# Optimization experiments

Hardware: AMD Instinct MI355X
Metric: run time of the kernel (lower is better)

## Reference

```python
import jax, jax.numpy as jnp
import numpy as np

EMB = 768
HEADS = 12
HEAD_DIM = EMB // HEADS

def setup_inputs() -> dict:
    key = jax.random.key(0)
    ks = jax.random.split(key, 5)
    B, T = 8, 1024
    x = jax.random.normal(ks[0], (B, T, EMB), dtype=jnp.float32)
    s = 1.0 / np.sqrt(EMB)
    W_attn = jax.random.normal(ks[1], (EMB, 3 * EMB), dtype=jnp.float32) * s
    b_attn = jax.random.normal(ks[2], (3 * EMB,), dtype=jnp.float32) * 0.02
    W_proj = jax.random.normal(ks[3], (EMB, EMB), dtype=jnp.float32) * s
    b_proj = jax.random.normal(ks[4], (EMB,), dtype=jnp.float32) * 0.02
    return {"x": x, "W_attn": W_attn, "b_attn": b_attn, "W_proj": W_proj, "b_proj": b_proj}

def reference(x, W_attn, b_attn, W_proj, b_proj):
    B, T, C = x.shape
    qkv = x @ W_attn + b_attn  # [B,T,3C]
    q, k, v = jnp.split(qkv, 3, axis=-1)
    # [B,H,T,d]
    q = q.reshape(B, T, HEADS, HEAD_DIM).transpose(0, 2, 1, 3)
    k = k.reshape(B, T, HEADS, HEAD_DIM).transpose(0, 2, 1, 3)
    v = v.reshape(B, T, HEADS, HEAD_DIM).transpose(0, 2, 1, 3)
    scores = jnp.einsum('bhqd,bhkd->bhqk', q, k) * (HEAD_DIM ** -0.5)
    causal = jnp.tril(jnp.ones((T, T), dtype=bool))
    scores = jnp.where(causal[None, None], scores, -jnp.inf)
    attn = jax.nn.softmax(scores, axis=-1)
    out = jnp.einsum('bhqk,bhkd->bhqd', attn, v)
    out = out.transpose(0, 2, 1, 3).reshape(B, T, C)
    return out @ W_proj + b_proj
```

## Files before the change

### kernel.cpp

```cpp
#include <hip/hip_runtime.h>
#include <hip/hip_bf16.h>
#include <math.h>

typedef __bf16 bf16;
typedef __attribute__((ext_vector_type(8))) __bf16 bf16x8;
typedef __attribute__((ext_vector_type(4))) short s16x4;
typedef __attribute__((ext_vector_type(4))) float f32x4;

#define EMB 768
#define T_SEQ 1024
#define HEADS 12
#define HDIM 64

__global__ void prep_k(const float* __restrict__ x, bf16* __restrict__ xb,
                       const float* __restrict__ Wa, bf16* __restrict__ Wta,
                       const float* __restrict__ Wp, bf16* __restrict__ Wtp) {
  __shared__ float tile[32][33];
  const int blk = blockIdx.x, tid = threadIdx.x;
  if (blk < 3072) {
    const size_t i = (size_t)blk * 256 + tid;
    const float4* p = (const float4*)(x + i * 8);
    const float4 a = p[0], b = p[1];
    bf16x8 v;
    v[0] = (bf16)a.x; v[1] = (bf16)a.y; v[2] = (bf16)a.z; v[3] = (bf16)a.w;
    v[4] = (bf16)b.x; v[5] = (bf16)b.y; v[6] = (bf16)b.z; v[7] = (bf16)b.w;
    *(bf16x8*)(xb + i * 8) = v;
    return;
  }
  const float* in;
  bf16* out;
  int C, t;
  if (blk < 3072 + 1728) { in = Wa; out = Wta; C = 3 * EMB; t = blk - 3072; }
  else                   { in = Wp; out = Wtp; C = EMB;     t = blk - 4800; }
  const int R = EMB;
  const int c0 = (t % (C / 32)) * 32, r0 = (t / (C / 32)) * 32;
  const int tx = tid & 31, ty = tid >> 5;
  for (int i = ty; i < 32; i += 8)
    tile[i][tx] = in[(size_t)(r0 + i) * C + c0 + tx];
  __syncthreads();
  for (int i = ty; i < 32; i += 8)
    out[(size_t)(c0 + i) * R + r0 + tx] = (bf16)tile[tx][i];
}

template <int MODE, int NXT>
__global__ __launch_bounds__(256) void gemm_bt(
    const bf16* __restrict__ A, const bf16* __restrict__ Bt, const float* __restrict__ bias,
    bf16* __restrict__ Cb, float* __restrict__ Cf, int M, int N, int K) {
  __shared__ __align__(16) bf16 As0[128 * 32];
  __shared__ __align__(16) bf16 As1[128 * 32];
  __shared__ __align__(16) bf16 Bs0[128 * 32];
  __shared__ __align__(16) bf16 Bs1[128 * 32];
  const int lane = threadIdx.x & 63;
  const int wave = threadIdx.x >> 6;
  const int quad = lane >> 4, lc = lane & 15;

  const int xcd = blockIdx.x & 7;
  const int idx = blockIdx.x >> 3;
  const int m0 = (xcd * 8 + (idx & 7)) * 128;
  const int n0 = (idx >> 3) * 128;

  const int wm = (wave >> 1) * 64, wn = (wave & 1) * 64;
  const int srow = lane >> 2;
  const int skk = (lane & 3) * 8;

  f32x4 zero = {0.f, 0.f, 0.f, 0.f};
  f32x4 acc[4][4];
#pragma unroll
  for (int i = 0; i < 4; ++i)
#pragma unroll
    for (int j = 0; j < 4; ++j) acc[i][j] = zero;

  for (int k0 = 0; k0 < K; k0 += 64) {
    __syncthreads();
#pragma unroll
    for (int c = wave; c < 8; c += 4) {
      const bf16* gA = A + (size_t)(m0 + c * 16 + srow) * K + k0 + skk;
      const bf16* gB = Bt + (size_t)(n0 + c * 16 + srow) * K + k0 + skk;
      __builtin_amdgcn_global_load_lds((const __attribute__((address_space(1))) void*)gA,
                                       (__attribute__((address_space(3))) void*)(As0 + c * 512), 16, 0, 0);
      __builtin_amdgcn_global_load_lds((const __attribute__((address_space(1))) void*)(gA + 32),
                                       (__attribute__((address_space(3))) void*)(As1 + c * 512), 16, 0, 0);
      __builtin_amdgcn_global_load_lds((const __attribute__((address_space(1))) void*)gB,
                                       (__attribute__((address_space(3))) void*)(Bs0 + c * 512), 16, 0, 0);
      __builtin_amdgcn_global_load_lds((const __attribute__((address_space(1))) void*)(gB + 32),
                                       (__attribute__((address_space(3))) void*)(Bs1 + c * 512), 16, 0, 0);
    }
    __syncthreads();
    {
      bf16x8 af[4], bfr[4];
#pragma unroll
      for (int t = 0; t < 4; ++t) af[t] = *(const bf16x8*)&As0[(wm + t * 16 + lc) * 32 + quad * 8];
#pragma unroll
      for (int t = 0; t < 4; ++t) bfr[t] = *(const bf16x8*)&Bs0[(wn + t * 16 + lc) * 32 + quad * 8];
#pragma unroll
      for (int tm = 0; tm < 4; ++tm)
#pragma unroll
        for (int tn = 0; tn < 4; ++tn)
          acc[tm][tn] = __builtin_amdgcn_mfma_f32_16x16x32_bf16(af[tm], bfr[tn], acc[tm][tn], 0, 0, 0);
    }
    {
      bf16x8 af[4], bfr[4];
#pragma unroll
      for (int t = 0; t < 4; ++t) af[t] = *(const bf16x8*)&As1[(wm + t * 16 + lc) * 32 + quad * 8];
#pragma unroll
      for (int t = 0; t < 4; ++t) bfr[t] = *(const bf16x8*)&Bs1[(wn + t * 16 + lc) * 32 + quad * 8];
#pragma unroll
      for (int tm = 0; tm < 4; ++tm)
#pragma unroll
        for (int tn = 0; tn < 4; ++tn)
          acc[tm][tn] = __builtin_amdgcn_mfma_f32_16x16x32_bf16(af[tm], bfr[tn], acc[tm][tn], 0, 0, 0);
    }
  }

#pragma unroll
  for (int tm = 0; tm < 4; ++tm) {
#pragma unroll
    for (int tn = 0; tn < 4; ++tn) {
      const int col = n0 + wn + tn * 16 + lc;
      const float bv = bias[col];
#pragma unroll
      for (int r = 0; r < 4; ++r) {
        const int row = m0 + wm + tm * 16 + quad * 4 + r;
        const float v = acc[tm][tn][r] + bv;
        if (MODE == 0) Cb[(size_t)row * N + col] = (bf16)v;
        else           Cf[(size_t)row * N + col] = v;
      }
    }
  }
}

__global__ __launch_bounds__(512, 4) void attn_k(const bf16* __restrict__ qkv,
                                                 bf16* __restrict__ outb) {
  __shared__ __align__(16) bf16 Qs[128][72];
  __shared__ __align__(16) bf16 Ks[128][72];
  __shared__ __align__(16) bf16 Vt[64][132];

  const int lane = threadIdx.x & 63;
  const int wave = threadIdx.x >> 6;
  const int quad = lane >> 4, lc = lane & 15;
  const int flat = blockIdx.x;
  const int bh = flat % (HEADS * 8);
  const int qt = 7 - flat / (HEADS * 8);
  const int h = bh % HEADS;
  const int b = bh / HEADS;
  const int q0 = qt * 128;
  const size_t rowB = (size_t)b * T_SEQ;
  const int hoff = h * HDIM;
  const int tid = threadIdx.x;
  const float C1 = 0.125f * 1.44269504f;

  for (int c = tid; c < 128 * 8; c += 512) {
    const int r = c >> 3, d8 = (c & 7) * 8;
    bf16x8 v = *(const bf16x8*)(qkv + (rowB + q0 + r) * (3 * EMB) + hoff + d8);
#pragma unroll
    for (int i = 0; i < 8; ++i) v[i] = (bf16)((float)v[i] * C1);
    *(bf16x8*)&Qs[r][d8] = v;
  }

  f32x4 zero = {0.f, 0.f, 0.f, 0.f};
  float l_run = 0.f;
  f32x4 o[4];
#pragma unroll
  for (int dt = 0; dt < 4; ++dt) o[dt] = zero;
  const int myq = q0 + wave * 16 + lc;

  for (int kt = 0; kt <= qt; ++kt) {
    const int kb = kt * 128;
    __syncthreads();
    for (int c = tid; c < 128 * 8; c += 512) {
      const int key = c >> 3, d8 = (c & 7) * 8;
      *(bf16x8*)&Ks[key][d8] =
          *(const bf16x8*)(qkv + (rowB + kb + key) * (3 * EMB) + EMB + hoff + d8);
    }
    for (int c = tid; c < 128 * 8; c += 512) {
      const int key = c >> 3, d8 = (c & 7) * 8;
      bf16x8 v = *(const bf16x8*)(qkv + (rowB + kb + key) * (3 * EMB) + 2 * EMB + hoff + d8);
#pragma unroll
      for (int i = 0; i < 8; ++i) Vt[d8 + i][key] = v[i];
    }
    __syncthreads();

    f32x4 s[8];
#pragma unroll
    for (int j = 0; j < 8; ++j) s[j] = zero;
#pragma unroll
    for (int ks = 0; ks < 2; ++ks) {
      bf16x8 bq = *(const bf16x8*)&Qs[wave * 16 + lc][ks * 32 + quad * 8];
#pragma unroll
      for (int j = 0; j < 8; ++j) {
        bf16x8 ak = *(const bf16x8*)&Ks[j * 16 + lc][ks * 32 + quad * 8];
        s[j] = __builtin_amdgcn_mfma_f32_16x16x32_bf16(ak, bq, s[j], 0, 0, 0);
      }
    }

    s16x4 pf[8];
    const bool diag = (kt == qt);
    if (diag) {
#pragma unroll
      for (int j = 0; j < 8; ++j) {
#pragma unroll
        for (int r = 0; r < 4; ++r) {
          const bool masked = (kb + j * 16 + quad * 4 + r > myq);
          const float p = masked ? 0.f : exp2f(s[j][r]);
          l_run += p;
          pf[j][r] = __builtin_bit_cast(short, (bf16)p);
        }
      }
    } else {
#pragma unroll
      for (int j = 0; j < 8; ++j) {
#pragma unroll
        for (int r = 0; r < 4; ++r) {
          const float p = exp2f(s[j][r]);
          l_run += p;
          pf[j][r] = __builtin_bit_cast(short, (bf16)p);
        }
      }
    }

#pragma unroll
    for (int j = 0; j < 8; ++j) {
#pragma unroll
      for (int dt = 0; dt < 4; ++dt) {
        s16x4 av = *(const s16x4*)&Vt[dt * 16 + lc][j * 16 + quad * 4];
        o[dt] = __builtin_amdgcn_mfma_f32_16x16x16bf16_1k(av, pf[j], o[dt], 0, 0, 0);
      }
    }
  }

  l_run += __shfl_xor(l_run, 16);
  l_run += __shfl_xor(l_run, 32);
  const float inv = 1.0f / l_run;
  __syncthreads();
#pragma unroll
  for (int dt = 0; dt < 4; ++dt)
#pragma unroll
    for (int r = 0; r < 4; ++r)
      Qs[wave * 16 + lc][dt * 16 + quad * 4 + r] = (bf16)(o[dt][r] * inv);
  __syncthreads();
  for (int c = tid; c < 128 * 8; c += 512) {
    const int r = c >> 3, d8 = (c & 7) * 8;
    *(bf16x8*)(outb + (rowB + q0 + r) * EMB + hoff + d8) = *(const bf16x8*)&Qs[r][d8];
  }
}

extern "C" void kernel_launch(void* const* d_in, const int* in_sizes, int n_in,
                              void* d_out, int out_size, void* d_ws, size_t ws_size,
                              hipStream_t stream) {
  const float* x = (const float*)d_in[0];
  const float* Wattn = (const float*)d_in[1];
  const float* battn = (const float*)d_in[2];
  const float* Wproj = (const float*)d_in[3];
  const float* bproj = (const float*)d_in[4];
  float* out = (float*)d_out;

  const int M = in_sizes[0] / EMB;
  const int Bn = M / T_SEQ;

  bf16* ws = (bf16*)d_ws;
  bf16* xb = ws;
  bf16* Wt_attn = xb + (size_t)M * EMB;
  bf16* Wt_proj = Wt_attn + (size_t)3 * EMB * EMB;
  bf16* qkv = Wt_proj + (size_t)EMB * EMB;
  bf16* attnb = qkv + (size_t)M * 3 * EMB;

  const int cvt_blocks = M * EMB / 8 / 256;
  prep_k<<<cvt_blocks + 1728 + 576, 256, 0, stream>>>(x, xb, Wattn, Wt_attn, Wproj, Wt_proj);

  gemm_bt<0, 18><<<18 * 64, 256, 0, stream>>>(
      xb, Wt_attn, battn, qkv, nullptr, M, 3 * EMB, EMB);

  attn_k<<<dim3((T_SEQ / 128) * Bn * HEADS), 512, 0, stream>>>(qkv, attnb);

  gemm_bt<1, 6><<<6 * 64, 256, 0, stream>>>(
      attnb, Wt_proj, bproj, nullptr, out, M, EMB, EMB);
}
```

Measured before the change: 180.1 us.

## Prefetch next K/V tile into registers and XOR-swizzle transposed V in LDS

The attention kernel now loads the next K and V tile from global memory into registers while the current tile is being computed, so global load latency overlaps with the MFMA work. The transposed V shared buffer drops its padded layout for an XOR swizzle on 4-key groups, which is meant to avoid bank conflicts on the scattered transpose writes and the MFMA reads. This adds register pressure (four extra bf16x8 vectors per thread) under launch bounds of 512 threads and 4 blocks, which could lower occupancy or cause spills.

```diff
diff --git a/kernel.cpp b/kernel.cpp
--- a/kernel.cpp
+++ b/kernel.cpp
@@ -133,7 +133,7 @@
                                                  bf16* __restrict__ outb) {
   __shared__ __align__(16) bf16 Qs[128][72];
   __shared__ __align__(16) bf16 Ks[128][72];
-  __shared__ __align__(16) bf16 Vt[64][132];
+  __shared__ __align__(16) bf16 Vt[64 * 128];
 
   const int lane = threadIdx.x & 63;
   const int wave = threadIdx.x >> 6;
@@ -149,6 +149,19 @@
   const int tid = threadIdx.x;
   const float C1 = 0.125f * 1.44269504f;
 
+  const int skey0 = tid >> 3;
+  const int sd8 = (tid & 7) * 8;
+  const bf16* kbase = qkv + (rowB)*3 * EMB + EMB + hoff;
+  const bf16* vbase = qkv + (rowB)*3 * EMB + 2 * EMB + hoff;
+
+  bf16x8 kreg[2], vreg[2];
+#pragma unroll
+  for (int t = 0; t < 2; ++t) {
+    const int key = skey0 + t * 64;
+    kreg[t] = *(const bf16x8*)(kbase + (size_t)key * (3 * EMB) + sd8);
+    vreg[t] = *(const bf16x8*)(vbase + (size_t)key * (3 * EMB) + sd8);
+  }
+
   for (int c = tid; c < 128 * 8; c += 512) {
     const int r = c >> 3, d8 = (c & 7) * 8;
     bf16x8 v = *(const bf16x8*)(qkv + (rowB + q0 + r) * (3 * EMB) + hoff + d8);
@@ -167,18 +180,28 @@
   for (int kt = 0; kt <= qt; ++kt) {
     const int kb = kt * 128;
     __syncthreads();
-    for (int c = tid; c < 128 * 8; c += 512) {
-      const int key = c >> 3, d8 = (c & 7) * 8;
-      *(bf16x8*)&Ks[key][d8] =
-          *(const bf16x8*)(qkv + (rowB + kb + key) * (3 * EMB) + EMB + hoff + d8);
-    }
-    for (int c = tid; c < 128 * 8; c += 512) {
-      const int key = c >> 3, d8 = (c & 7) * 8;
-      bf16x8 v = *(const bf16x8*)(qkv + (rowB + kb + key) * (3 * EMB) + 2 * EMB + hoff + d8);
-#pragma unroll
-      for (int i = 0; i < 8; ++i) Vt[d8 + i][key] = v[i];
+#pragma unroll
+    for (int t = 0; t < 2; ++t) {
+      const int key = skey0 + t * 64;
+      *(bf16x8*)&Ks[key][sd8] = kreg[t];
+      const int kg = key >> 2, kl = key & 3;
+#pragma unroll
+      for (int i = 0; i < 8; ++i) {
+        const int d = sd8 + i;
+        Vt[d * 128 + (((kg ^ (d & 31)) << 2) | kl)] = vreg[t][i];
+      }
     }
     __syncthreads();
+
+    if (kt < qt) {
+      const int nb = (kt + 1) * 128;
+#pragma unroll
+      for (int t = 0; t < 2; ++t) {
+        const int key = nb + skey0 + t * 64;
+        kreg[t] = *(const bf16x8*)(kbase + (size_t)key * (3 * EMB) + sd8);
+        vreg[t] = *(const bf16x8*)(vbase + (size_t)key * (3 * EMB) + sd8);
+      }
+    }
 
     f32x4 s[8];
 #pragma unroll
@@ -222,7 +245,8 @@
     for (int j = 0; j < 8; ++j) {
 #pragma unroll
       for (int dt = 0; dt < 4; ++dt) {
-        s16x4 av = *(const s16x4*)&Vt[dt * 16 + lc][j * 16 + quad * 4];
+        const int d = dt * 16 + lc;
+        s16x4 av = *(const s16x4*)&Vt[d * 128 + (((j * 4 + quad) ^ (d & 31)) << 2)];
         o[dt] = __builtin_amdgcn_mfma_f32_16x16x16bf16_1k(av, pf[j], o[dt], 0, 0, 0);
       }
     }
```

After: 184.1 us. 2.2% more time.
